# Kernel tuning notes

Measured on AMD Instinct MI355X. Metric: run time of the kernel, lower is better.

The kernel has to match this reference:

```python
import jax, jax.numpy as jnp
import numpy as np

NUM_CLASSES = 10
OUT_DIM = 16
NUM_ROUTING = 3
ROUTING_BIAS = 0.1


def _squash(s):
    # s: [B, C, D]; norm over last (out_capsule) dim, matches torch norm(dim=2)
    norm = jnp.linalg.norm(s, axis=2, keepdims=True)
    # s / (1+norm^2) / norm * norm^2 == s * norm / (1 + norm^2)
    return s * norm / (1.0 + norm * norm)


def setup_inputs() -> dict:
    key = jax.random.key(0)
    k1, k2 = jax.random.split(key)
    B, N, IN_DIM = 256, 2304, 8
    x = jax.random.normal(k1, (B, N, IN_DIM), dtype=jnp.float32)
    # kaiming-normal-ish init for W [N, in_dim, classes*out_dim]
    W = jax.random.normal(k2, (N, IN_DIM, NUM_CLASSES * OUT_DIM), dtype=jnp.float32) * np.sqrt(2.0 / IN_DIM)
    return {"x": x, "W": W}


def reference(x, W):
    B, N, _ = x.shape
    # broadcast-multiply+sum in original == per-capsule matmul
    u_hat = jnp.einsum('bni,nio->bno', x, W).reshape(B, N, NUM_CLASSES, OUT_DIM)
    u_hat_sg = jax.lax.stop_gradient(u_hat)
    b = jnp.zeros((B, N, NUM_CLASSES), dtype=x.dtype)
    v = None
    for i in range(NUM_ROUTING):
        c = jax.nn.softmax(b, axis=2)  # [B, N, C]
        if i == NUM_ROUTING - 1:
            s = jnp.einsum('bnc,bncd->bcd', c, u_hat) + ROUTING_BIAS
            v = _squash(s)
        else:
            s = jnp.einsum('bnc,bncd->bcd', c, u_hat_sg) + ROUTING_BIAS
            # NOTE: original updates b with pre-squash s (not v) -- kept faithful
            b = b + jnp.einsum('bncd,bcd->bnc', u_hat_sg, s)
    return v
```

## Files before the change

kernel.cpp:

```cpp
#include <hip/hip_runtime.h>
#include <math.h>

#define B_TOT   256
#define N_TOT   2304
#define IN_DIM  8
#define NC      10
#define OD      16
#define CD      160
#define RBIAS   0.1f

#define BTILE    64
#define NS       192
#define NPB      (N_TOT / NS)
#define NTHREADS 640
#define XR       (NPB * IN_DIM + 4)
#define LB       72
#define NF4      (B_TOT * CD / 4)
#define RSUB     4
#define YSUB     (NS / RSUB)

template <int FIRST>
__global__ __launch_bounds__(NTHREADS) void routing_round(
    const float* __restrict__ x,
    const float* __restrict__ W,
    const float* __restrict__ S_acc,
    float* __restrict__ part)
{
    __shared__ float sh_x[BTILE * XR];
    __shared__ float sh_lg[2][NC * LB];

    const int tid = threadIdx.x;
    const int b0  = blockIdx.x * BTILE;
    const int n0  = blockIdx.y * NPB;
    const int b   = tid & 63;
    const int cu  = __builtin_amdgcn_readfirstlane(tid >> 6);

    {
        const int XT4 = BTILE * (NPB * IN_DIM / 4);
        for (int k = tid; k < XT4; k += NTHREADS) {
            int bb   = k / (NPB * 2);
            int off4 = k - bb * (NPB * 2);
            float4 v = *(const float4*)(x + ((size_t)(b0 + bb) * N_TOT + n0) * IN_DIM + off4 * 4);
            *(float4*)(&sh_x[bb * XR + off4 * 4]) = v;
        }
    }

    float S[OD];
    if (!FIRST) {
        const float4* sp = (const float4*)(S_acc + (size_t)(b0 + b) * CD + cu * OD);
        #pragma unroll
        for (int q = 0; q < 4; q++) ((float4*)S)[q] = sp[q];
    }

    float acc[OD];
    #pragma unroll
    for (int d = 0; d < OD; d++) acc[d] = 0.f;

    __syncthreads();

    const float* Wc = W + cu * OD;

    for (int nn = 0; nn < NPB; nn++) {
        float xf[IN_DIM];
        {
            const float4* xp = (const float4*)(&sh_x[b * XR + nn * IN_DIM]);
            ((float4*)xf)[0] = xp[0];
            ((float4*)xf)[1] = xp[1];
        }

        const float* Wn = Wc + (size_t)(n0 + nn) * (IN_DIM * CD);
        float u[OD];
        #pragma unroll
        for (int d = 0; d < OD; d++) u[d] = xf[0] * Wn[d];
        #pragma unroll
        for (int i = 1; i < IN_DIM; i++) {
            const float* Wi = Wn + i * CD;
            #pragma unroll
            for (int d = 0; d < OD; d++) u[d] = fmaf(xf[i], Wi[d], u[d]);
        }

        if (!FIRST) {
            const int cur = nn & 1;
            float lg = 0.f;
            #pragma unroll
            for (int d = 0; d < OD; d++) lg = fmaf(u[d], S[d], lg);
            sh_lg[cur][cu * LB + b] = lg;
            __syncthreads();

            float m = -1e30f;
            float row[NC];
            #pragma unroll
            for (int k = 0; k < NC; k++) {
                row[k] = sh_lg[cur][k * LB + b];
                m = fmaxf(m, row[k]);
            }
            float den = 0.f;
            #pragma unroll
            for (int k = 0; k < NC; k++) den += __expf(row[k] - m);
            float cw = __expf(lg - m) / den;

            #pragma unroll
            for (int d = 0; d < OD; d++) acc[d] = fmaf(cw, u[d], acc[d]);
        } else {
            #pragma unroll
            for (int d = 0; d < OD; d++) acc[d] += u[d];
        }
    }

    float* dst = part + ((size_t)blockIdx.y * B_TOT + (b0 + b)) * CD + cu * OD;
    #pragma unroll
    for (int q = 0; q < 4; q++)
        ((float4*)dst)[q] = ((float4*)acc)[q];
}

__global__ __launch_bounds__(1024) void reduce_round(
    const float* __restrict__ part,
    float* __restrict__ S_acc,
    float* __restrict__ v_out,
    float scale, int round)
{
    __shared__ float4 sh[RSUB][256];

    const int gl  = threadIdx.x & 255;
    const int sub = threadIdx.x >> 8;
    const int g   = blockIdx.x * 256 + gl;

    const float4* p4 = (const float4*)part + (size_t)sub * YSUB * NF4 + g;
    float4 s = { 0.f, 0.f, 0.f, 0.f };
    #pragma unroll 4
    for (int y = 0; y < YSUB; y++) {
        float4 t = p4[(size_t)y * NF4];
        s.x += t.x; s.y += t.y; s.z += t.z; s.w += t.w;
    }
    sh[sub][gl] = s;
    __syncthreads();

    if (threadIdx.x < 256) {
        float4 a = sh[0][gl], b = sh[1][gl], c = sh[2][gl], d = sh[3][gl];
        float4 t = { a.x + b.x + c.x + d.x,
                     a.y + b.y + c.y + d.y,
                     a.z + b.z + c.z + d.z,
                     a.w + b.w + c.w + d.w };
        t.x = t.x * scale + RBIAS;
        t.y = t.y * scale + RBIAS;
        t.z = t.z * scale + RBIAS;
        t.w = t.w * scale + RBIAS;

        if (round == 0) {
            ((float4*)S_acc)[g] = t;
        } else if (round == 1) {
            float4 o = ((float4*)S_acc)[g];
            o.x += t.x; o.y += t.y; o.z += t.z; o.w += t.w;
            ((float4*)S_acc)[g] = o;
        } else {
            float ss = t.x * t.x + t.y * t.y + t.z * t.z + t.w * t.w;
            ss += __shfl_xor(ss, 1, 64);
            ss += __shfl_xor(ss, 2, 64);
            float norm = sqrtf(ss);
            float k2 = norm / (1.0f + ss);
            float4 v = { t.x * k2, t.y * k2, t.z * k2, t.w * k2 };
            ((float4*)v_out)[g] = v;
        }
    }
}

extern "C" void kernel_launch(void* const* d_in, const int* in_sizes, int n_in,
                              void* d_out, int out_size, void* d_ws, size_t ws_size,
                              hipStream_t stream) {
    const float* x = (const float*)d_in[0];
    const float* W = (const float*)d_in[1];
    float* out = (float*)d_out;

    float* part  = (float*)d_ws;
    float* S_acc = part + (size_t)NS * B_TOT * CD;

    const dim3 rgrid(B_TOT / BTILE, NS);
    const int  RG = NF4 / 256;

    routing_round<1><<<rgrid, NTHREADS, 0, stream>>>(x, W, S_acc, part);
    reduce_round<<<RG, 1024, 0, stream>>>(part, S_acc, out, 0.1f, 0);

    routing_round<0><<<rgrid, NTHREADS, 0, stream>>>(x, W, S_acc, part);
    reduce_round<<<RG, 1024, 0, stream>>>(part, S_acc, out, 1.0f, 1);

    routing_round<0><<<rgrid, NTHREADS, 0, stream>>>(x, W, S_acc, part);
    reduce_round<<<RG, 1024, 0, stream>>>(part, S_acc, out, 1.0f, 2);
}
```

Measured before the change: 224.2 us.

## Spread partial-sum reduction across more, smaller blocks to fill the GPU

Measured after the change: 212.4 us. -5.3%, faster.

```diff
diff --git a/kernel.cpp b/kernel.cpp
--- a/kernel.cpp
+++ b/kernel.cpp
@@ -16,8 +16,9 @@
 #define XR       (NPB * IN_DIM + 4)
 #define LB       72
 #define NF4      (B_TOT * CD / 4)
-#define RSUB     4
-#define YSUB     (NS / RSUB)
+#define RCOLS    32
+#define RGRPS    8
+#define RYPER    (NS / RGRPS)
 
 template <int FIRST>
 __global__ __launch_bounds__(NTHREADS) void routing_round(
@@ -113,34 +114,35 @@
         ((float4*)dst)[q] = ((float4*)acc)[q];
 }
 
-__global__ __launch_bounds__(1024) void reduce_round(
+__global__ __launch_bounds__(256) void reduce_round(
     const float* __restrict__ part,
     float* __restrict__ S_acc,
     float* __restrict__ v_out,
     float scale, int round)
 {
-    __shared__ float4 sh[RSUB][256];
+    __shared__ float4 sh[RGRPS][RCOLS];
 
-    const int gl  = threadIdx.x & 255;
-    const int sub = threadIdx.x >> 8;
-    const int g   = blockIdx.x * 256 + gl;
+    const int col = threadIdx.x & (RCOLS - 1);
+    const int grp = threadIdx.x >> 5;
+    const int g   = blockIdx.x * RCOLS + col;
 
-    const float4* p4 = (const float4*)part + (size_t)sub * YSUB * NF4 + g;
+    const float4* p4 = (const float4*)part + (size_t)grp * NF4 + g;
     float4 s = { 0.f, 0.f, 0.f, 0.f };
     #pragma unroll 4
-    for (int y = 0; y < YSUB; y++) {
-        float4 t = p4[(size_t)y * NF4];
+    for (int y = 0; y < RYPER; y++) {
+        float4 t = p4[(size_t)y * RGRPS * NF4];
         s.x += t.x; s.y += t.y; s.z += t.z; s.w += t.w;
     }
-    sh[sub][gl] = s;
+    sh[grp][col] = s;
     __syncthreads();
 
-    if (threadIdx.x < 256) {
-        float4 a = sh[0][gl], b = sh[1][gl], c = sh[2][gl], d = sh[3][gl];
-        float4 t = { a.x + b.x + c.x + d.x,
-                     a.y + b.y + c.y + d.y,
-                     a.z + b.z + c.z + d.z,
-                     a.w + b.w + c.w + d.w };
+    if (threadIdx.x < RCOLS) {
+        float4 t = { 0.f, 0.f, 0.f, 0.f };
+        #pragma unroll
+        for (int k = 0; k < RGRPS; k++) {
+            float4 q = sh[k][col];
+            t.x += q.x; t.y += q.y; t.z += q.z; t.w += q.w;
+        }
         t.x = t.x * scale + RBIAS;
         t.y = t.y * scale + RBIAS;
         t.z = t.z * scale + RBIAS;
@@ -175,14 +177,14 @@
     float* S_acc = part + (size_t)NS * B_TOT * CD;
 
     const dim3 rgrid(B_TOT / BTILE, NS);
-    const int  RG = NF4 / 256;
+    const int  RG = NF4 / RCOLS;
 
     routing_round<1><<<rgrid, NTHREADS, 0, stream>>>(x, W, S_acc, part);
-    reduce_round<<<RG, 1024, 0, stream>>>(part, S_acc, out, 0.1f, 0);
+    reduce_round<<<RG, 256, 0, stream>>>(part, S_acc, out, 0.1f, 0);
 
     routing_round<0><<<rgrid, NTHREADS, 0, stream>>>(x, W, S_acc, part);
-    reduce_round<<<RG, 1024, 0, stream>>>(part, S_acc, out, 1.0f, 1);
+    reduce_round<<<RG, 256, 0, stream>>>(part, S_acc, out, 1.0f, 1);
 
     routing_round<0><<<rgrid, NTHREADS, 0, stream>>>(x, W, S_acc, part);
-    reduce_round<<<RG, 1024, 0, stream>>>(part, S_acc, out, 1.0f, 2);
+    reduce_round<<<RG, 256, 0, stream>>>(part, S_acc, out, 1.0f, 2);
 }
```
